# Kernel tuning notes

Hardware: AMD Instinct MI355X
Metric: run time of the kernel (lower is better)

## Reference

```python
import jax, jax.numpy as jnp
import numpy as np

N_GRAPHS = 500
CHAIN = 200
D_STATE = 64
HID = 128
NEG_SLOPE = 0.2  # PyG GATConv default


def setup_inputs() -> dict:
    key = jax.random.key(0)
    ks = jax.random.split(key, 9)
    N = N_GRAPHS * CHAIN
    # batched bidirectional chain graphs (as in create_chain_graph_batch)
    off = np.arange(N_GRAPHS, dtype=np.int32) * CHAIN
    a = (off[:, None] + np.arange(CHAIN - 1, dtype=np.int32)[None, :]).ravel()
    b = a + 1
    edge_index = jnp.asarray(np.stack([np.concatenate([a, b]), np.concatenate([b, a])]), dtype=jnp.int32)
    x = jax.random.normal(ks[0], (N, D_STATE), jnp.float32)
    s1 = 1.0 / np.sqrt(D_STATE)
    W1 = jax.random.normal(ks[1], (D_STATE, 2 * HID), jnp.float32) * s1
    att_src1 = jax.random.normal(ks[2], (2, HID), jnp.float32) * (1.0 / np.sqrt(HID))
    att_dst1 = jax.random.normal(ks[3], (2, HID), jnp.float32) * (1.0 / np.sqrt(HID))
    b1 = jnp.zeros((2 * HID,), jnp.float32)
    s2 = 1.0 / np.sqrt(2 * HID)
    W2 = jax.random.normal(ks[4], (2 * HID, HID), jnp.float32) * s2
    att_src2 = jax.random.normal(ks[5], (1, HID), jnp.float32) * (1.0 / np.sqrt(HID))
    att_dst2 = jax.random.normal(ks[6], (1, HID), jnp.float32) * (1.0 / np.sqrt(HID))
    b2 = jnp.zeros((HID,), jnp.float32)
    return {"x": x, "edge_index": edge_index, "W1": W1, "att_src1": att_src1,
            "att_dst1": att_dst1, "b1": b1, "W2": W2, "att_src2": att_src2,
            "att_dst2": att_dst2, "b2": b2}


def gat_conv(x, src, dst, W, att_src, att_dst, bias, concat):
    # PyG GATConv: per-head linear, additive attention, segment softmax over dst
    N = x.shape[0]
    H, C = att_src.shape
    h = (x @ W).reshape(N, H, C)                          # [N,H,C]
    a_s = (h * att_src).sum(-1)                           # [N,H]
    a_d = (h * att_dst).sum(-1)                           # [N,H]
    logits = jax.nn.leaky_relu(a_s[src] + a_d[dst], NEG_SLOPE)  # [E,H]
    m = jax.ops.segment_max(logits, dst, num_segments=N)
    e = jnp.exp(logits - m[dst])
    s = jax.ops.segment_sum(e, dst, num_segments=N)
    alpha = e / (s[dst] + 1e-16)                          # [E,H]
    out = jax.ops.segment_sum(h[src] * alpha[:, :, None], dst, num_segments=N)  # [N,H,C]
    out = out.reshape(N, H * C) if concat else out.mean(axis=1)
    return out + bias


def reference(x, edge_index, W1, att_src1, att_dst1, b1, W2, att_src2, att_dst2, b2):
    N = x.shape[0]
    loop = jnp.arange(N, dtype=edge_index.dtype)
    src = jnp.concatenate([edge_index[0], loop])  # add_self_loops=True (PyG default)
    dst = jnp.concatenate([edge_index[1], loop])
    h = gat_conv(x, src, dst, W1, att_src1, att_dst1, b1, concat=True)
    h = jax.nn.gelu(h, approximate=False)  # torch F.gelu default = exact erf
    h = gat_conv(h, src, dst, W2, att_src2, att_dst2, b2, concat=False)
    return jax.nn.gelu(h, approximate=False)
```

## Files before the change

### kernel.cpp

```cpp
#include <hip/hip_runtime.h>
#include <hip/hip_bf16.h>

#define NG 500
#define CH 200
#define NN (NG*CH)
#define DS 64
#define HDIM 128
#define C1 256
#define NEG_SLOPE 0.2f
#define GB 1563

typedef unsigned short ushort_t;
typedef __attribute__((ext_vector_type(8))) short bf16x8;
typedef __attribute__((ext_vector_type(4))) float f32x4;

__device__ __forceinline__ float us2f(ushort_t u){
  union { unsigned int i; float f; } v; v.i = ((unsigned int)u) << 16; return v.f;
}
__device__ __forceinline__ ushort_t f2us(float f){
  union { float f; unsigned int i; } v; v.f = f;
  unsigned int x = v.i;
  return (ushort_t)((x + 0x7fffu + ((x >> 16) & 1u)) >> 16);
}
__device__ __forceinline__ unsigned int cvt_pk_bf16(float a, float b){
  unsigned int r;
  asm("v_cvt_pk_bf16_f32 %0, %1, %2" : "=v"(r) : "v"(a), "v"(b));
  return r;
}
__device__ __forceinline__ float lrelu(float v){ return v > 0.f ? v : NEG_SLOPE * v; }
__device__ __forceinline__ float gelu_fast(float x){
  float x2 = x * x;
  float zn = x * fmaf(-0.0713548163f, x2, -1.5957691216f);
  float e  = __expf(zn);
  return x * __builtin_amdgcn_rcpf(1.f + e);
}

__global__ void prep_w(const void* __restrict__ x,
                       const void* W1, const void* as1, const void* ad1, const void* b1,
                       const void* W2, const void* as2, const void* ad2, const void* b2,
                       int* __restrict__ flag,
                       ushort_t* w1t, ushort_t* w2t,
                       float* b1f, float* b2f,
                       ushort_t* wsd1, ushort_t* wsd2)
{
  __shared__ int cnt;
  if (threadIdx.x == 0) cnt = 0;
  __syncthreads();
  {
    const ushort_t* p = (const ushort_t*)x;
    int local = 0;
    for (int i = threadIdx.x; i < 8192; i += 256) {
      float v = us2f(p[i]);
      if (!(fabsf(v) < 100.f)) local++;
    }
    atomicAdd(&cnt, local);
  }
  __syncthreads();
  const bool F = cnt > 16;
  if (blockIdx.x == 0 && threadIdx.x == 0) flag[0] = F ? 1 : 0;

  int i = blockIdx.x * 256 + threadIdx.x;
  #define LD(p, j) (F ? ((const float*)(p))[j] : us2f(((const ushort_t*)(p))[j]))
  if (i < 16384)      { int k = i >> 8, n = i & 255; w1t[n*64  + k] = f2us(LD(W1, i)); }
  else if (i < 49152) { int j = i - 16384, k = j >> 7, n = j & 127; w2t[n*256 + k] = f2us(LD(W2, j)); }
  else if (i < 49408) { b1f[i-49152] = LD(b1, i-49152); }
  else if (i < 49536) { b2f[i-49408] = LD(b2, i-49408); }
  else if (i < 53632) {
    int j = i - 49536, dot = j >> 4, lsub = j & 15;
    int k = dot >> 2, c = dot & 3, head = c >> 1;
    const void* av = (c & 1) ? ad1 : as1;
    float s = 0.f;
    #pragma unroll
    for (int jj = 0; jj < 8; jj++) {
      int cc = lsub*8 + jj;
      s += LD(W1, k*256 + head*128 + cc) * LD(av, head*128 + cc);
    }
    s += __shfl_xor(s, 1, 64); s += __shfl_xor(s, 2, 64);
    s += __shfl_xor(s, 4, 64); s += __shfl_xor(s, 8, 64);
    if (lsub == 0) {
      ushort_t hi = f2us(s);
      wsd1[c*64 + k] = hi;
      wsd1[(c+4)*64 + k] = f2us(s - us2f(hi));
    }
  }
  else if (i < 61824) {
    int j = i - 53632, dot = j >> 4, lsub = j & 15;
    int k = dot >> 1, c = dot & 1;
    const void* av = c ? ad2 : as2;
    float s = 0.f;
    #pragma unroll
    for (int jj = 0; jj < 8; jj++) {
      int cc = lsub*8 + jj;
      s += LD(W2, k*128 + cc) * LD(av, cc);
    }
    s += __shfl_xor(s, 1, 64); s += __shfl_xor(s, 2, 64);
    s += __shfl_xor(s, 4, 64); s += __shfl_xor(s, 8, 64);
    if (lsub == 0) {
      ushort_t hi = f2us(s);
      wsd2[c*256 + k] = hi;
      wsd2[(c+2)*256 + k] = f2us(s - us2f(hi));
    }
  }
  else if (i < 62336) { wsd1[512  + (i - 61824)] = 0; }
  else if (i < 65408) { wsd2[1024 + (i - 62336)] = 0; }
  #undef LD
}

__global__ __launch_bounds__(256, 4) void fused(
    const int* __restrict__ flag, const void* __restrict__ x,
    const ushort_t* __restrict__ w1t, const ushort_t* __restrict__ w2t,
    const ushort_t* __restrict__ wsd1, const ushort_t* __restrict__ wsd2,
    const float* __restrict__ b1f, const float* __restrict__ b2f,
    void* __restrict__ out)
{
  __shared__ ushort_t lds[17952];
  __shared__ float scratch[800];
  ushort_t* As  = lds;
  ushort_t* g1L = lds;

  const int t  = threadIdx.x;
  const int m0 = blockIdx.x * 64;
  const int l = t & 63, w = t >> 6;
  const int ln = l & 15, quad = l >> 4;
  const bool F = flag[0] != 0;

  #pragma unroll
  for (int i = 0; i < 5; i++) {
    int q = t + i*256;
    int r = q >> 4, off = (q & 15) * 4;
    int gr = m0 - 2 + r;
    if (r < 68 && gr >= 0 && gr < NN) {
      if (F) {
        float4 xv = *(const float4*)(&((const float*)x)[(size_t)gr*DS + off]);
        uint2 u; u.x = cvt_pk_bf16(xv.x, xv.y); u.y = cvt_pk_bf16(xv.z, xv.w);
        *(uint2*)(&As[r*72 + off]) = u;
      } else {
        *(ushort4*)(&As[r*72 + off]) = *(const ushort4*)(&((const ushort_t*)x)[(size_t)gr*DS + off]);
      }
    } else {
      ushort4 z = {0,0,0,0};
      *(ushort4*)(&As[r*72 + off]) = z;
    }
  }

  f32x4 acc[5][4];
  #pragma unroll
  for (int mi = 0; mi < 5; mi++)
    #pragma unroll
    for (int nj = 0; nj < 4; nj++) acc[mi][nj] = (f32x4){0.f,0.f,0.f,0.f};
  f32x4 acc_att[5];
  #pragma unroll
  for (int mi = 0; mi < 5; mi++) acc_att[mi] = (f32x4){0.f,0.f,0.f,0.f};

  __syncthreads();
  #pragma unroll
  for (int h = 0; h < 2; h++) {
    #pragma unroll
    for (int ks = 0; ks < 2; ks++) {
      const int kk = ks*32 + quad*8;
      bf16x8 a[5], b[2];
      #pragma unroll
      for (int njl = 0; njl < 2; njl++)
        b[njl] = *(const bf16x8*)(&w1t[(w*64 + h*32 + njl*16 + ln)*64 + kk]);
      #pragma unroll
      for (int mi = 0; mi < 5; mi++) a[mi] = *(const bf16x8*)(&As[(mi*16 + ln)*72 + kk]);
      #pragma unroll
      for (int mi = 0; mi < 5; mi++)
        #pragma unroll
        for (int njl = 0; njl < 2; njl++)
          acc[mi][2*h+njl] = __builtin_amdgcn_mfma_f32_16x16x32_bf16(a[mi], b[njl], acc[mi][2*h+njl], 0, 0, 0);
      if (h == 0 && w == 0) {
        bf16x8 batt = *(const bf16x8*)(&wsd1[ln*64 + kk]);
        #pragma unroll
        for (int mi = 0; mi < 5; mi++)
          acc_att[mi] = __builtin_amdgcn_mfma_f32_16x16x32_bf16(a[mi], batt, acc_att[mi], 0, 0, 0);
      }
    }
  }

  if (w == 0) {
    #pragma unroll
    for (int mi = 0; mi < 5; mi++)
      #pragma unroll
      for (int r = 0; r < 4; r++) {
        float v = acc_att[mi][r];
        float vc = v + __shfl(v, (l + 4) & 63, 64);
        int row = mi*16 + quad*4 + r;
        if (ln < 4 && row < 68) scratch[ln*68 + row] = vc;
      }
  }
  __syncthreads();

  if (t < 132) {
    int hh = (t >= 66) ? 1 : 0;
    int n  = t - 66*hh;
    int gj = m0 - 1 + n;
    int p  = gj % CH;
    const float* Sa = &scratch[(2*hh)*68];
    const float* Da = &scratch[(2*hh+1)*68];
    float ad = Da[n+1], as_s = Sa[n+1], as_l = Sa[n], as_r = Sa[n+2];
    bool hl = p > 0, hr = p < CH-1;
    float zs = lrelu(as_s + ad);
    float zl = hl ? lrelu(as_l + ad) : -1e30f;
    float zr = hr ? lrelu(as_r + ad) : -1e30f;
    float mx = fmaxf(zs, fmaxf(zl, zr));
    float el = hl ? __expf(zl - mx) : 0.f;
    float es = __expf(zs - mx);
    float er = hr ? __expf(zr - mx) : 0.f;
    float inv = __builtin_amdgcn_rcpf(el + es + er + 1e-16f);
    scratch[272 + n*8 + hh*4 + 0] = el*inv;
    scratch[272 + n*8 + hh*4 + 1] = es*inv;
    scratch[272 + n*8 + hh*4 + 2] = er*inv;
  }
  __syncthreads();

  {
    float b1v[4];
    #pragma unroll
    for (int nj = 0; nj < 4; nj++) b1v[nj] = b1f[w*64 + nj*16 + ln];
    if (t < 128) {
      int rr = (t < 64) ? 0 : 67;
      int c4 = (t & 63) * 4;
      ushort4 z = {0,0,0,0};
      *(ushort4*)(&g1L[rr*264 + c4]) = z;
    }
    const int head = w >> 1;
    #pragma unroll
    for (int mi = 0; mi < 5; mi++) {
      const int mip = (mi < 4) ? mi+1 : 4;
      const int mim = (mi > 0) ? mi-1 : 0;
      float hp3[4], hm0[4];
      #pragma unroll
      for (int nj = 0; nj < 4; nj++) {
        float up_a = __shfl(acc[mi ][nj][0], (l+16)&63, 64);
        float up_b = __shfl(acc[mip][nj][0], (l+16)&63, 64);
        float dn_a = __shfl(acc[mi ][nj][3], (l-16)&63, 64);
        float dn_b = __shfl(acc[mim][nj][3], (l-16)&63, 64);
        hp3[nj] = (quad < 3) ? up_a : up_b;
        hm0[nj] = (quad > 0) ? dn_a : dn_b;
      }
      #pragma unroll
      for (int r = 0; r < 4; r++) {
        int row = mi*16 + quad*4 + r;
        if (row >= 1 && row <= 66) {
          float4 av = *(const float4*)(&scratch[272 + (row-1)*8 + head*4]);
          float o[4];
          #pragma unroll
          for (int nj = 0; nj < 4; nj++) {
            float self = acc[mi][nj][r];
            float hm = (r > 0) ? acc[mi][nj][r-1] : hm0[nj];
            float hp = (r < 3) ? acc[mi][nj][r+1] : hp3[nj];
            o[nj] = gelu_fast(av.y*self + av.x*hm + av.z*hp + b1v[nj]);
          }
          unsigned int u01 = cvt_pk_bf16(o[0], o[1]);
          unsigned int u23 = cvt_pk_bf16(o[2], o[3]);
          ushort_t* base = &g1L[row*264 + w*64 + ln];
          base[0]  = (ushort_t)u01; base[16] = (ushort_t)(u01 >> 16);
          base[32] = (ushort_t)u23; base[48] = (ushort_t)(u23 >> 16);
        }
      }
    }
  }
  __syncthreads();

  f32x4 acc2[5][2];
  #pragma unroll
  for (int mi = 0; mi < 5; mi++)
    #pragma unroll
    for (int nj = 0; nj < 2; nj++) acc2[mi][nj] = (f32x4){0.f,0.f,0.f,0.f};
  f32x4 acc2_att[5];
  #pragma unroll
  for (int mi = 0; mi < 5; mi++) acc2_att[mi] = (f32x4){0.f,0.f,0.f,0.f};

  #pragma unroll
  for (int ck = 0; ck < 4; ck++) {
    bf16x8 a2[2][5];
    #pragma unroll
    for (int ks = 0; ks < 2; ks++)
      #pragma unroll
      for (int mi = 0; mi < 5; mi++) {
        int ar = mi*16 + ln;
        if (mi == 4) ar = (ar < 67) ? ar : 67;
        a2[ks][mi] = *(const bf16x8*)(&g1L[ar*264 + ck*64 + ks*32 + quad*8]);
      }
    if (ck == w) {
      #pragma unroll
      for (int ks = 0; ks < 2; ks++) {
        bf16x8 batt2 = *(const bf16x8*)(&wsd2[ln*256 + ck*64 + ks*32 + quad*8]);
        #pragma unroll
        for (int mi = 0; mi < 5; mi++)
          acc2_att[mi] = __builtin_amdgcn_mfma_f32_16x16x32_bf16(a2[ks][mi], batt2, acc2_att[mi], 0, 0, 0);
      }
    }
    #pragma unroll
    for (int h2 = 0; h2 < 2; h2++) {
      #pragma unroll
      for (int ks = 0; ks < 2; ks++) {
        bf16x8 b = *(const bf16x8*)(&w2t[(w*32 + h2*16 + ln)*256 + ck*64 + ks*32 + quad*8]);
        #pragma unroll
        for (int mi = 0; mi < 5; mi++)
          acc2[mi][h2] = __builtin_amdgcn_mfma_f32_16x16x32_bf16(a2[ks][mi], b, acc2[mi][h2], 0, 0, 0);
      }
    }
  }

  #pragma unroll
  for (int mi = 0; mi < 5; mi++)
    #pragma unroll
    for (int r = 0; r < 4; r++) {
      float v = acc2_att[mi][r];
      float vc = v + __shfl(v, (l + 2) & 63, 64);
      int row = mi*16 + quad*4 + r;
      if (ln < 2 && row < 68) scratch[(w*2 + ln)*68 + row] = vc;
    }
  __syncthreads();

  if (t < 64) {
    int gi = m0 + t;
    if (gi < NN) {
      int p = gi % CH;
      float ad = 0.f, as_s = 0.f, as_l = 0.f, as_r = 0.f;
      #pragma unroll
      for (int ww = 0; ww < 4; ww++) {
        as_s += scratch[(ww*2)*68 + t+2];
        as_l += scratch[(ww*2)*68 + t+1];
        as_r += scratch[(ww*2)*68 + t+3];
        ad   += scratch[(ww*2+1)*68 + t+2];
      }
      bool hl = p > 0, hr = p < CH-1;
      float zs = lrelu(as_s + ad);
      float zl = hl ? lrelu(as_l + ad) : -1e30f;
      float zr = hr ? lrelu(as_r + ad) : -1e30f;
      float mx = fmaxf(zs, fmaxf(zl, zr));
      float el = hl ? __expf(zl - mx) : 0.f;
      float es = __expf(zs - mx);
      float er = hr ? __expf(zr - mx) : 0.f;
      float inv = __builtin_amdgcn_rcpf(el + es + er + 1e-16f);
      scratch[544 + t*4 + 0] = el*inv;
      scratch[544 + t*4 + 1] = es*inv;
      scratch[544 + t*4 + 2] = er*inv;
    }
  }
  __syncthreads();

  {
    float b2v[2];
    #pragma unroll
    for (int nj = 0; nj < 2; nj++) b2v[nj] = b2f[w*32 + nj*16 + ln];
    #pragma unroll
    for (int mi = 0; mi < 5; mi++) {
      const int mip = (mi < 4) ? mi+1 : 4;
      const int mim = (mi > 0) ? mi-1 : 0;
      float hp3[2], hm0[2];
      #pragma unroll
      for (int nj = 0; nj < 2; nj++) {
        float up_a = __shfl(acc2[mi ][nj][0], (l+16)&63, 64);
        float up_b = __shfl(acc2[mip][nj][0], (l+16)&63, 64);
        float dn_a = __shfl(acc2[mi ][nj][3], (l-16)&63, 64);
        float dn_b = __shfl(acc2[mim][nj][3], (l-16)&63, 64);
        hp3[nj] = (quad < 3) ? up_a : up_b;
        hm0[nj] = (quad > 0) ? dn_a : dn_b;
      }
      #pragma unroll
      for (int r = 0; r < 4; r++) {
        int row = mi*16 + quad*4 + r;
        if (row >= 2 && row <= 65) {
          int n = row - 2;
          int gi = m0 + n;
          if (gi < NN) {
            float4 av = *(const float4*)(&scratch[544 + n*4]);
            float o0, o1;
            {
              float self = acc2[mi][0][r];
              float hm = (r > 0) ? acc2[mi][0][r-1] : hm0[0];
              float hp = (r < 3) ? acc2[mi][0][r+1] : hp3[0];
              o0 = gelu_fast(av.y*self + av.x*hm + av.z*hp + b2v[0]);
            }
            {
              float self = acc2[mi][1][r];
              float hm = (r > 0) ? acc2[mi][1][r-1] : hm0[1];
              float hp = (r < 3) ? acc2[mi][1][r+1] : hp3[1];
              o1 = gelu_fast(av.y*self + av.x*hm + av.z*hp + b2v[1]);
            }
            int c2 = w*32 + ln;
            if (F) {
              ((float*)out)[(size_t)gi*HDIM + c2]      = o0;
              ((float*)out)[(size_t)gi*HDIM + c2 + 16] = o1;
            } else {
              unsigned int u = cvt_pk_bf16(o0, o1);
              ((ushort_t*)out)[(size_t)gi*HDIM + c2]      = (ushort_t)u;
              ((ushort_t*)out)[(size_t)gi*HDIM + c2 + 16] = (ushort_t)(u >> 16);
            }
          }
        }
      }
    }
  }
}

extern "C" void kernel_launch(void* const* d_in, const int* in_sizes, int n_in,
                              void* d_out, int out_size, void* d_ws, size_t ws_size,
                              hipStream_t stream)
{
  const void* x   = d_in[0];
  const void* W1  = d_in[2];
  const void* as1 = d_in[3];
  const void* ad1 = d_in[4];
  const void* b1  = d_in[5];
  const void* W2  = d_in[6];
  const void* as2 = d_in[7];
  const void* ad2 = d_in[8];
  const void* b2  = d_in[9];

  char* w = (char*)d_ws;
  size_t off = 0;
  int* flag = (int*)w;                       off += 256;
  ushort_t* w1t = (ushort_t*)(w + off);      off += 64 * 256 * 2;
  ushort_t* w2t = (ushort_t*)(w + off);      off += 256 * 128 * 2;
  float* b1f    = (float*)(w + off);         off += 256 * 4;
  float* b2f    = (float*)(w + off);         off += 128 * 4;
  ushort_t* wsd1 = (ushort_t*)(w + off);     off += 16 * 64 * 2;
  ushort_t* wsd2 = (ushort_t*)(w + off);     off += 16 * 256 * 2;

  prep_w<<<256, 256, 0, stream>>>(x, W1, as1, ad1, b1, W2, as2, ad2, b2,
                                  flag, w1t, w2t, b1f, b2f, wsd1, wsd2);
  fused<<<GB, 256, 0, stream>>>(flag, x, w1t, w2t, wsd1, wsd2, b1f, b2f, d_out);
}
```

Before: 159.5 us.

## Fold weight preprocessing into fused kernel, dropping prep launch

Removes the separate prep_w kernel. Every block of the fused kernel now runs the dtype-detection scan, computes the attention projection vectors into shared memory, and reads W1/W2 directly from the original layout with strided scalar loads and bf16 conversion. This removes one kernel launch and the dependency on the workspace. In exchange, all 1563 blocks repeat the preprocessing work (an 8192-element scan and 128-length dot products per thread), and the weight fragment loads become uncoalesced. It also uses more LDS, which may reduce occupancy.

```diff
diff --git a/kernel.cpp b/kernel.cpp
--- a/kernel.cpp
+++ b/kernel.cpp
@@ -35,86 +35,19 @@
   return x * __builtin_amdgcn_rcpf(1.f + e);
 }
 
-__global__ void prep_w(const void* __restrict__ x,
-                       const void* W1, const void* as1, const void* ad1, const void* b1,
-                       const void* W2, const void* as2, const void* ad2, const void* b2,
-                       int* __restrict__ flag,
-                       ushort_t* w1t, ushort_t* w2t,
-                       float* b1f, float* b2f,
-                       ushort_t* wsd1, ushort_t* wsd2)
-{
-  __shared__ int cnt;
-  if (threadIdx.x == 0) cnt = 0;
-  __syncthreads();
-  {
-    const ushort_t* p = (const ushort_t*)x;
-    int local = 0;
-    for (int i = threadIdx.x; i < 8192; i += 256) {
-      float v = us2f(p[i]);
-      if (!(fabsf(v) < 100.f)) local++;
-    }
-    atomicAdd(&cnt, local);
-  }
-  __syncthreads();
-  const bool F = cnt > 16;
-  if (blockIdx.x == 0 && threadIdx.x == 0) flag[0] = F ? 1 : 0;
-
-  int i = blockIdx.x * 256 + threadIdx.x;
-  #define LD(p, j) (F ? ((const float*)(p))[j] : us2f(((const ushort_t*)(p))[j]))
-  if (i < 16384)      { int k = i >> 8, n = i & 255; w1t[n*64  + k] = f2us(LD(W1, i)); }
-  else if (i < 49152) { int j = i - 16384, k = j >> 7, n = j & 127; w2t[n*256 + k] = f2us(LD(W2, j)); }
-  else if (i < 49408) { b1f[i-49152] = LD(b1, i-49152); }
-  else if (i < 49536) { b2f[i-49408] = LD(b2, i-49408); }
-  else if (i < 53632) {
-    int j = i - 49536, dot = j >> 4, lsub = j & 15;
-    int k = dot >> 2, c = dot & 3, head = c >> 1;
-    const void* av = (c & 1) ? ad1 : as1;
-    float s = 0.f;
-    #pragma unroll
-    for (int jj = 0; jj < 8; jj++) {
-      int cc = lsub*8 + jj;
-      s += LD(W1, k*256 + head*128 + cc) * LD(av, head*128 + cc);
-    }
-    s += __shfl_xor(s, 1, 64); s += __shfl_xor(s, 2, 64);
-    s += __shfl_xor(s, 4, 64); s += __shfl_xor(s, 8, 64);
-    if (lsub == 0) {
-      ushort_t hi = f2us(s);
-      wsd1[c*64 + k] = hi;
-      wsd1[(c+4)*64 + k] = f2us(s - us2f(hi));
-    }
-  }
-  else if (i < 61824) {
-    int j = i - 53632, dot = j >> 4, lsub = j & 15;
-    int k = dot >> 1, c = dot & 1;
-    const void* av = c ? ad2 : as2;
-    float s = 0.f;
-    #pragma unroll
-    for (int jj = 0; jj < 8; jj++) {
-      int cc = lsub*8 + jj;
-      s += LD(W2, k*128 + cc) * LD(av, cc);
-    }
-    s += __shfl_xor(s, 1, 64); s += __shfl_xor(s, 2, 64);
-    s += __shfl_xor(s, 4, 64); s += __shfl_xor(s, 8, 64);
-    if (lsub == 0) {
-      ushort_t hi = f2us(s);
-      wsd2[c*256 + k] = hi;
-      wsd2[(c+2)*256 + k] = f2us(s - us2f(hi));
-    }
-  }
-  else if (i < 62336) { wsd1[512  + (i - 61824)] = 0; }
-  else if (i < 65408) { wsd2[1024 + (i - 62336)] = 0; }
-  #undef LD
-}
-
 __global__ __launch_bounds__(256, 4) void fused(
-    const int* __restrict__ flag, const void* __restrict__ x,
-    const ushort_t* __restrict__ w1t, const ushort_t* __restrict__ w2t,
-    const ushort_t* __restrict__ wsd1, const ushort_t* __restrict__ wsd2,
-    const float* __restrict__ b1f, const float* __restrict__ b2f,
+    const void* __restrict__ x,
+    const void* __restrict__ W1, const void* __restrict__ as1,
+    const void* __restrict__ ad1, const void* __restrict__ b1,
+    const void* __restrict__ W2, const void* __restrict__ as2,
+    const void* __restrict__ ad2, const void* __restrict__ b2,
     void* __restrict__ out)
 {
   __shared__ ushort_t lds[17952];
+  __shared__ ushort_t wsd1S[16*64];
+  __shared__ ushort_t wsd2S[16*256];
   __shared__ float scratch[800];
+  __shared__ int cnt;
   ushort_t* As  = lds;
   ushort_t* g1L = lds;
 
@@ -122,7 +55,22 @@
   const int m0 = blockIdx.x * 64;
   const int l = t & 63, w = t >> 6;
   const int ln = l & 15, quad = l >> 4;
-  const bool F = flag[0] != 0;
+
+  if (t == 0) cnt = 0;
+  __syncthreads();
+  {
+    const ushort_t* p = (const ushort_t*)x;
+    int local = 0;
+    for (int i = t; i < 8192; i += 256) {
+      float v = us2f(p[i]);
+      if (!(fabsf(v) < 100.f)) local++;
+    }
+    atomicAdd(&cnt, local);
+  }
+  __syncthreads();
+  const bool F = cnt > 16;
+
+  #define LD(p, j) (F ? ((const float*)(p))[j] : us2f(((const ushort_t*)(p))[j]))
 
   #pragma unroll
   for (int i = 0; i < 5; i++) {
@@ -143,6 +91,38 @@
     }
   }
 
+  {
+    int k = t >> 2, c = t & 3, head = c >> 1;
+    const void* av = (c & 1) ? ad1 : as1;
+    float s = 0.f;
+    #pragma unroll 8
+    for (int cc = 0; cc < 128; cc++)
+      s += LD(W1, k*256 + head*128 + cc) * LD(av, head*128 + cc);
+    ushort_t hi = f2us(s);
+    wsd1S[c*64 + k] = hi;
+    wsd1S[(c+4)*64 + k] = f2us(s - us2f(hi));
+  }
+  #pragma unroll
+  for (int dd = 0; dd < 2; dd++) {
+    int d = t + dd*256;
+    int k = d >> 1, c = d & 1;
+    const void* av = c ? ad2 : as2;
+    float s = 0.f;
+    #pragma unroll 8
+    for (int cc = 0; cc < 128; cc++)
+      s += LD(W2, k*128 + cc) * LD(av, cc);
+    ushort_t hi = f2us(s);
+    wsd2S[c*256 + k] = hi;
+    wsd2S[(c+2)*256 + k] = f2us(s - us2f(hi));
+  }
+  {
+    ushort4 z = {0,0,0,0};
+    if (t < 128) *(ushort4*)(&wsd1S[512 + t*4]) = z;
+    #pragma unroll
+    for (int i = 0; i < 3; i++)
+      *(ushort4*)(&wsd2S[1024 + (t + i*256)*4]) = z;
+  }
+
   f32x4 acc[5][4];
   #pragma unroll
   for (int mi = 0; mi < 5; mi++)
@@ -153,6 +133,7 @@
   for (int mi = 0; mi < 5; mi++) acc_att[mi] = (f32x4){0.f,0.f,0.f,0.f};
 
   __syncthreads();
+
   #pragma unroll
   for (int h = 0; h < 2; h++) {
     #pragma unroll
@@ -160,8 +141,26 @@
       const int kk = ks*32 + quad*8;
       bf16x8 a[5], b[2];
       #pragma unroll
-      for (int njl = 0; njl < 2; njl++)
-        b[njl] = *(const bf16x8*)(&w1t[(w*64 + h*32 + njl*16 + ln)*64 + kk]);
+      for (int njl = 0; njl < 2; njl++) {
+        const int c = w*64 + h*32 + njl*16 + ln;
+        union { uint4 u; bf16x8 v; } cv;
+        if (F) {
+          const float* Wf = (const float*)W1;
+          float f0 = Wf[(kk+0)*256 + c], f1 = Wf[(kk+1)*256 + c];
+          float f2 = Wf[(kk+2)*256 + c], f3 = Wf[(kk+3)*256 + c];
+          float f4 = Wf[(kk+4)*256 + c], f5 = Wf[(kk+5)*256 + c];
+          float f6 = Wf[(kk+6)*256 + c], f7 = Wf[(kk+7)*256 + c];
+          cv.u.x = cvt_pk_bf16(f0, f1); cv.u.y = cvt_pk_bf16(f2, f3);
+          cv.u.z = cvt_pk_bf16(f4, f5); cv.u.w = cvt_pk_bf16(f6, f7);
+        } else {
+          const ushort_t* Wu = (const ushort_t*)W1;
+          cv.u.x = (unsigned)Wu[(kk+0)*256+c] | ((unsigned)Wu[(kk+1)*256+c] << 16);
+          cv.u.y = (unsigned)Wu[(kk+2)*256+c] | ((unsigned)Wu[(kk+3)*256+c] << 16);
+          cv.u.z = (unsigned)Wu[(kk+4)*256+c] | ((unsigned)Wu[(kk+5)*256+c] << 16);
+          cv.u.w = (unsigned)Wu[(kk+6)*256+c] | ((unsigned)Wu[(kk+7)*256+c] << 16);
+        }
+        b[njl] = cv.v;
+      }
       #pragma unroll
       for (int mi = 0; mi < 5; mi++) a[mi] = *(const bf16x8*)(&As[(mi*16 + ln)*72 + kk]);
       #pragma unroll
@@ -170,7 +169,7 @@
         for (int njl = 0; njl < 2; njl++)
           acc[mi][2*h+njl] = __builtin_amdgcn_mfma_f32_16x16x32_bf16(a[mi], b[njl], acc[mi][2*h+njl], 0, 0, 0);
       if (h == 0 && w == 0) {
-        bf16x8 batt = *(const bf16x8*)(&wsd1[ln*64 + kk]);
+        bf16x8 batt = *(const bf16x8*)(&wsd1S[ln*64 + kk]);
         #pragma unroll
         for (int mi = 0; mi < 5; mi++)
           acc_att[mi] = __builtin_amdgcn_mfma_f32_16x16x32_bf16(a[mi], batt, acc_att[mi], 0, 0, 0);
@@ -217,7 +216,7 @@
   {
     float b1v[4];
     #pragma unroll
-    for (int nj = 0; nj < 4; nj++) b1v[nj] = b1f[w*64 + nj*16 + ln];
+    for (int nj = 0; nj < 4; nj++) b1v[nj] = LD(b1, w*64 + nj*16 + ln);
     if (t < 128) {
       int rr = (t < 64) ? 0 : 67;
       int c4 = (t & 63) * 4;
@@ -286,7 +285,7 @@
     if (ck == w) {
       #pragma unroll
       for (int ks = 0; ks < 2; ks++) {
-        bf16x8 batt2 = *(const bf16x8*)(&wsd2[ln*256 + ck*64 + ks*32 + quad*8]);
+        bf16x8 batt2 = *(const bf16x8*)(&wsd2S[ln*256 + ck*64 + ks*32 + quad*8]);
         #pragma unroll
         for (int mi = 0; mi < 5; mi++)
           acc2_att[mi] = __builtin_amdgcn_mfma_f32_16x16x32_bf16(a2[ks][mi], batt2, acc2_att[mi], 0, 0, 0);
@@ -296,10 +295,27 @@
     for (int h2 = 0; h2 < 2; h2++) {
       #pragma unroll
       for (int ks = 0; ks < 2; ks++) {
-        bf16x8 b = *(const bf16x8*)(&w2t[(w*32 + h2*16 + ln)*256 + ck*64 + ks*32 + quad*8]);
+        const int kk = ck*64 + ks*32 + quad*8;
+        const int c = w*32 + h2*16 + ln;
+        union { uint4 u; bf16x8 v; } cv;
+        if (F) {
+          const float* Wf = (const float*)W2;
+          float f0 = Wf[(kk+0)*128 + c], f1 = Wf[(kk+1)*128 + c];
+          float f2 = Wf[(kk+2)*128 + c], f3 = Wf[(kk+3)*128 + c];
+          float f4 = Wf[(kk+4)*128 + c], f5 = Wf[(kk+5)*128 + c];
+          float f6 = Wf[(kk+6)*128 + c], f7 = Wf[(kk+7)*128 + c];
+          cv.u.x = cvt_pk_bf16(f0, f1); cv.u.y = cvt_pk_bf16(f2, f3);
+          cv.u.z = cvt_pk_bf16(f4, f5); cv.u.w = cvt_pk_bf16(f6, f7);
+        } else {
+          const ushort_t* Wu = (const ushort_t*)W2;
+          cv.u.x = (unsigned)Wu[(kk+0)*128+c] | ((unsigned)Wu[(kk+1)*128+c] << 16);
+          cv.u.y = (unsigned)Wu[(kk+2)*128+c] | ((unsigned)Wu[(kk+3)*128+c] << 16);
+          cv.u.z = (unsigned)Wu[(kk+4)*128+c] | ((unsigned)Wu[(kk+5)*128+c] << 16);
+          cv.u.w = (unsigned)Wu[(kk+6)*128+c] | ((unsigned)Wu[(kk+7)*128+c] << 16);
+        }
         #pragma unroll
         for (int mi = 0; mi < 5; mi++)
-          acc2[mi][h2] = __builtin_amdgcn_mfma_f32_16x16x32_bf16(a2[ks][mi], b, acc2[mi][h2], 0, 0, 0);
+          acc2[mi][h2] = __builtin_amdgcn_mfma_f32_16x16x32_bf16(a2[ks][mi], cv.v, acc2[mi][h2], 0, 0, 0);
       }
     }
   }
@@ -346,7 +362,7 @@
   {
     float b2v[2];
     #pragma unroll
-    for (int nj = 0; nj < 2; nj++) b2v[nj] = b2f[w*32 + nj*16 + ln];
+    for (int nj = 0; nj < 2; nj++) b2v[nj] = LD(b2, w*32 + nj*16 + ln);
     #pragma unroll
     for (int mi = 0; mi < 5; mi++) {
       const int mip = (mi < 4) ? mi+1 : 4;
@@ -396,6 +412,7 @@
       }
     }
   }
+  #undef LD
 }
 
 extern "C" void kernel_launch(void* const* d_in, const int* in_sizes, int n_in,
@@ -411,18 +428,7 @@
   const void* as2 = d_in[7];
   const void* ad2 = d_in[8];
   const void* b2  = d_in[9];
-
-  char* w = (char*)d_ws;
-  size_t off = 0;
-  int* flag = (int*)w;                       off += 256;
-  ushort_t* w1t = (ushort_t*)(w + off);      off += 64 * 256 * 2;
-  ushort_t* w2t = (ushort_t*)(w + off);      off += 256 * 128 * 2;
-  float* b1f    = (float*)(w + off);         off += 256 * 4;
-  float* b2f    = (float*)(w + off);         off += 128 * 4;
-  ushort_t* wsd1 = (ushort_t*)(w + off);     off += 16 * 64 * 2;
-  ushort_t* wsd2 = (ushort_t*)(w + off);     off += 16 * 256 * 2;
-
-  prep_w<<<256, 256, 0, stream>>>(x, W1, as1, ad1, b1, W2, as2, ad2, b2,
-                                  flag, w1t, w2t, b1f, b2f, wsd1, wsd2);
-  fused<<<GB, 256, 0, stream>>>(flag, x, w1t, w2t, wsd1, wsd2, b1f, b2f, d_out);
-}
+  (void)d_ws; (void)ws_size;
+
+  fused<<<GB, 256, 0, stream>>>(x, W1, as1, ad1, b1, W2, as2, ad2, b2, d_out);
+}
```

After: 514.0 us. 3.22x slower.
